# Optimization experiments

Measured on AMD Instinct MI355X. Metric: run time of the kernel, lower is better.

Reference implementation:

```python
import jax, jax.numpy as jnp
import numpy as np

N = 100000   # nodes of type 'A'
D = 128      # embedding_dim and input feature dim
E = 1600000  # edges per metapath (avg degree 16)
R = 2        # metapaths with head type 'A'; beta has R+1 channels (self)


def setup_inputs() -> dict:
    key = jax.random.key(0)
    ks = jax.random.split(key, 8)
    s = 1.0 / np.sqrt(D)
    return {
        "x": jax.random.normal(ks[0], (N, D), jnp.float32),
        "edge_index_r1": jax.random.randint(ks[1], (2, E), 0, N),
        "edge_index_r2": jax.random.randint(ks[2], (2, E), 0, N),
        "W_lin": jax.random.normal(ks[3], (D, D), jnp.float32) * s,
        "b_lin": jnp.zeros((D,), jnp.float32),
        "W_conv": jax.random.normal(ks[4], (R + 1, D), jnp.float32) * s,  # kernel-size-1 Conv1d == linear
        "b_conv": jnp.zeros((R + 1,), jnp.float32),
        "attn_l_w": jax.random.normal(ks[5], (R, D), jnp.float32) * s,
        "attn_l_b": jnp.zeros((R,), jnp.float32),
        "attn_r_w": jax.random.normal(ks[6], (R, D), jnp.float32) * s,
        "attn_r_b": jnp.zeros((R,), jnp.float32),
        "alpha_weights": jnp.ones((R,), jnp.float32),
    }


def _segment_softmax(logits, seg, n):
    mx = jax.ops.segment_max(logits, seg, num_segments=n)
    mx = jnp.where(jnp.isfinite(mx), mx, 0.0)  # empty segments
    ex = jnp.exp(logits - mx[seg])
    denom = jax.ops.segment_sum(ex, seg, num_segments=n)
    return ex / (denom[seg] + 1e-16)


def reference(x, edge_index_r1, edge_index_r2, W_lin, b_lin, W_conv, b_conv,
              attn_l_w, attn_l_b, attn_r_w, attn_r_b, alpha_weights):
    n = x.shape[0]
    h = x @ W_lin.T + b_lin                              # get_h_dict: Linear
    beta = jax.nn.softmax(x @ W_conv.T + b_conv, axis=1)  # [N, R+1] relation weights
    al = x @ jnp.zeros((0,)) if False else h @ attn_l_w.T + attn_l_b  # [N, R]
    ar = h @ attn_r_w.T + attn_r_b                        # [N, R]
    rels = []
    for m, ei in enumerate((edge_index_r1, edge_index_r2)):
        dst, src = ei[0], ei[1]  # flow='target_to_source': aggregate into edge_index[0]
        logit = alpha_weights[m] * (al[src, m] + ar[dst, m])  # [E]
        att = _segment_softmax(logit, dst, n)
        rels.append(jax.ops.segment_sum(h[src] * att[:, None], dst, num_segments=n))
    rel = jnp.stack(rels + [h], axis=1)                   # [N, R+1, D], last slot = self
    out = jnp.einsum("nrd,nr->nd", rel, beta)            # matmul(perm, beta).squeeze
    return jax.nn.relu(out)                               # activation='relu'
```

## Files before the change

kernel.cpp:

```cpp
#include <hip/hip_runtime.h>

#define DIM 128
#define NSL 128
#define WMAX 25000

typedef __attribute__((ext_vector_type(8))) short bf16x8;
typedef __attribute__((ext_vector_type(4))) float f32x4;

__device__ __forceinline__ unsigned bfbits(float f) {
    unsigned u = __float_as_uint(f);
    return (u + 0x7FFFu + ((u >> 16) & 1u)) >> 16;
}
__device__ __forceinline__ float bflo(unsigned u) { return __uint_as_float(u << 16); }
__device__ __forceinline__ float bfhi(unsigned u) { return __uint_as_float(u & 0xFFFF0000u); }

__global__ __launch_bounds__(256) void k_gemm_h(
    const float* __restrict__ x, const float* __restrict__ W,
    const float* __restrict__ b, const float* __restrict__ Wc,
    const float* __restrict__ bcv, const float* __restrict__ alw,
    const float* __restrict__ alb, const float* __restrict__ alpha,
    unsigned short* __restrict__ h2u, float* __restrict__ exal0,
    float* __restrict__ exal1, float* __restrict__ betab, int n)
{
    __shared__ short wlds[128 * 136];
    __shared__ short xlds[64 * 136];
    const int tid  = threadIdx.x;
    const int row0 = blockIdx.x * 64;

    {
        const int j = tid >> 1, half = tid & 1;
        const float4* W4 = (const float4*)W;
#pragma unroll
        for (int i = 0; i < 8; ++i) {
            float4 fa = W4[j * 32 + half * 16 + i * 2];
            float4 fb = W4[j * 32 + half * 16 + i * 2 + 1];
            uint4 p;
            p.x = bfbits(fa.x) | (bfbits(fa.y) << 16);
            p.y = bfbits(fa.z) | (bfbits(fa.w) << 16);
            p.z = bfbits(fb.x) | (bfbits(fb.y) << 16);
            p.w = bfbits(fb.z) | (bfbits(fb.w) << 16);
            *(uint4*)&wlds[j * 136 + half * 64 + i * 8] = p;
        }
    }
    {
        const int r = tid >> 2, q = tid & 3;
        const int row = min(row0 + r, n - 1);
        const float4* x4 = (const float4*)x;
#pragma unroll
        for (int i = 0; i < 4; ++i) {
            float4 fa = x4[(size_t)row * 32 + q * 8 + i * 2];
            float4 fb = x4[(size_t)row * 32 + q * 8 + i * 2 + 1];
            uint4 p;
            p.x = bfbits(fa.x) | (bfbits(fa.y) << 16);
            p.y = bfbits(fa.z) | (bfbits(fa.w) << 16);
            p.z = bfbits(fb.x) | (bfbits(fb.y) << 16);
            p.w = bfbits(fb.z) | (bfbits(fb.w) << 16);
            *(uint4*)&xlds[r * 136 + q * 32 + i * 8] = p;
        }
    }
    __syncthreads();

    const int wv = tid >> 6, lane = tid & 63;
    const int lr = lane & 15, lg = lane >> 4;

    f32x4 acc[8];
#pragma unroll
    for (int c = 0; c < 8; ++c) acc[c] = (f32x4){0.f, 0.f, 0.f, 0.f};

#pragma unroll
    for (int ks = 0; ks < 4; ++ks) {
        bf16x8 a = *(const bf16x8*)&xlds[(wv * 16 + lr) * 136 + ks * 32 + lg * 8];
#pragma unroll
        for (int c = 0; c < 8; ++c) {
            bf16x8 bb = *(const bf16x8*)&wlds[(c * 16 + lr) * 136 + ks * 32 + lg * 8];
            acc[c] = __builtin_amdgcn_mfma_f32_16x16x32_bf16(a, bb, acc[c], 0, 0, 0);
        }
    }

    const int rl0 = wv * 16 + lg * 4;
    float as0[4] = {0.f,0.f,0.f,0.f}, as1[4] = {0.f,0.f,0.f,0.f};
#pragma unroll
    for (int c = 0; c < 8; ++c) {
        const int col = c * 16 + lr;
        const float bc = b[col];
        const float w0 = alw[col], w1 = alw[128 + col];
#pragma unroll
        for (int r = 0; r < 4; ++r) {
            const float hv = acc[c][r] + bc;
            const int row = row0 + rl0 + r;
            if (row < n)
                h2u[(size_t)row * DIM + col] = (unsigned short)bfbits(hv);
            as0[r] = fmaf(hv, w0, as0[r]);
            as1[r] = fmaf(hv, w1, as1[r]);
        }
    }
    float xs0[4] = {0.f,0.f,0.f,0.f}, xs1[4] = {0.f,0.f,0.f,0.f},
          xs2[4] = {0.f,0.f,0.f,0.f};
#pragma unroll
    for (int i = 0; i < 8; ++i) {
        const int col = lr + i * 16;
        const float wc0 = Wc[col], wc1 = Wc[128 + col], wc2 = Wc[256 + col];
#pragma unroll
        for (int r = 0; r < 4; ++r) {
            const float xv = bflo((unsigned)(unsigned short)xlds[(rl0 + r) * 136 + col]);
            xs0[r] = fmaf(xv, wc0, xs0[r]);
            xs1[r] = fmaf(xv, wc1, xs1[r]);
            xs2[r] = fmaf(xv, wc2, xs2[r]);
        }
    }
#pragma unroll
    for (int o = 1; o <= 8; o <<= 1) {
#pragma unroll
        for (int r = 0; r < 4; ++r) {
            as0[r] += __shfl_xor(as0[r], o);
            as1[r] += __shfl_xor(as1[r], o);
            xs0[r] += __shfl_xor(xs0[r], o);
            xs1[r] += __shfl_xor(xs1[r], o);
            xs2[r] += __shfl_xor(xs2[r], o);
        }
    }
    if (lr == 0) {
        const float a0 = alpha[0], a1 = alpha[1];
        const float ab0 = alb[0], ab1 = alb[1];
        const float b0 = bcv[0], b1 = bcv[1], b2 = bcv[2];
#pragma unroll
        for (int r = 0; r < 4; ++r) {
            const int row = row0 + rl0 + r;
            if (row < n) {
                exal0[row] = __expf(a0 * (as0[r] + ab0));
                exal1[row] = __expf(a1 * (as1[r] + ab1));
                float c0 = xs0[r] + b0, c1 = xs1[r] + b1, c2 = xs2[r] + b2;
                float mx = fmaxf(c0, fmaxf(c1, c2));
                float e0 = __expf(c0 - mx), e1 = __expf(c1 - mx),
                      e2 = __expf(c2 - mx);
                float s = e0 + e1 + e2;
                betab[row * 3 + 0] = e0 / s;
                betab[row * 3 + 1] = e1 / s;
                betab[row * 3 + 2] = e2 / s;
            }
        }
    }
}

__global__ __launch_bounds__(1024) void k_hist(
    const int* __restrict__ ei1, const int* __restrict__ ei2,
    unsigned* __restrict__ pb, unsigned char* __restrict__ ph, int n, int e)
{
    __shared__ unsigned lds[WMAX];
    const int blk = blockIdx.x;
    const int s   = blk % NSL;
    const int m   = blk / NSL;
    const int* ei = m ? ei2 : ei1;
    const int W   = (n + 3) >> 2;

    for (int i = threadIdx.x; i < W; i += 1024) lds[i] = 0;
    __syncthreads();

    const int sl = (e + NSL - 1) / NSL;
    const int j0 = s * sl, j1 = min(j0 + sl, e);
    for (int j = j0 + threadIdx.x; j < j1; j += 1024) {
        int d  = ei[j];
        int sh = (d & 3) * 8;
        unsigned old = atomicAdd(&lds[d >> 2], 1u << sh);
        ph[(size_t)m * e + j] = (unsigned char)((old >> sh) & 0xFF);
    }
    __syncthreads();

    unsigned* dst = pb + (size_t)blk * WMAX;
    for (int i = threadIdx.x; i < W; i += 1024) dst[i] = lds[i];
}

__global__ __launch_bounds__(256) void k_combine(
    unsigned* __restrict__ pb, int* __restrict__ cnt, int n)
{
    const int W = (n + 3) >> 2;
    int t = blockIdx.x * 256 + threadIdx.x;
    if (t >= 2 * W) return;
    const int m = t / W, w = t % W;

    unsigned run = 0;
    unsigned* base = pb + ((size_t)m * NSL) * WMAX + w;
    for (int s = 0; s < NSL; ++s) {
        unsigned v = base[(size_t)s * WMAX];
        base[(size_t)s * WMAX] = run;
        run += v;
    }
    int bin = 4 * w;
    if (bin + 3 < n) {
        int4 c = make_int4(run & 0xFF, (run >> 8) & 0xFF,
                           (run >> 16) & 0xFF, (run >> 24) & 0xFF);
        *(int4*)&cnt[m * n + bin] = c;
    } else {
        for (int j = 0; j < 4 && bin + j < n; ++j)
            cnt[m * n + bin + j] = (run >> (8 * j)) & 0xFF;
    }
}

__global__ __launch_bounds__(256) void k_scan1(
    const int* __restrict__ cnt, int* __restrict__ excl,
    int* __restrict__ bsum, int n2)
{
    __shared__ int sh[256];
    int t = threadIdx.x;
    int base = blockIdx.x * 1024 + t * 4;
    int v0 = (base + 0 < n2) ? cnt[base + 0] : 0;
    int v1 = (base + 1 < n2) ? cnt[base + 1] : 0;
    int v2 = (base + 2 < n2) ? cnt[base + 2] : 0;
    int v3 = (base + 3 < n2) ? cnt[base + 3] : 0;
    int s1 = v0 + v1, s2 = s1 + v2, s3 = s2 + v3;
    sh[t] = s3;
    __syncthreads();
    for (int off = 1; off < 256; off <<= 1) {
        int a = (t >= off) ? sh[t - off] : 0;
        __syncthreads();
        sh[t] += a;
        __syncthreads();
    }
    int eb = sh[t] - s3;
    if (t == 255) bsum[blockIdx.x] = sh[255];
    if (base + 0 < n2) excl[base + 0] = eb;
    if (base + 1 < n2) excl[base + 1] = eb + v0;
    if (base + 2 < n2) excl[base + 2] = eb + s1;
    if (base + 3 < n2) excl[base + 3] = eb + s2;
}

__global__ __launch_bounds__(256) void k_scan2(int* __restrict__ bsum, int nb)
{
    __shared__ int sh[256];
    int t = threadIdx.x;
    int v = (t < nb) ? bsum[t] : 0;
    sh[t] = v;
    __syncthreads();
    for (int off = 1; off < 256; off <<= 1) {
        int a = (t >= off) ? sh[t - off] : 0;
        __syncthreads();
        sh[t] += a;
        __syncthreads();
    }
    if (t < nb) bsum[t] = sh[t] - v;
}

__global__ __launch_bounds__(256) void k_scan3(
    int* __restrict__ rp, const int* __restrict__ bsum, int n2, int etot)
{
    int i = blockIdx.x * 256 + threadIdx.x;
    if (i < n2) rp[i] += bsum[i >> 10];
    if (i == 0) rp[n2] = etot;
}

__global__ __launch_bounds__(256) void k_fill(
    const int* __restrict__ ei1, const int* __restrict__ ei2,
    const unsigned char* __restrict__ ph, const unsigned* __restrict__ pb,
    const int* __restrict__ rp, int* __restrict__ srcs,
    int sl, int n, int e)
{
    int t = blockIdx.x * 256 + threadIdx.x;
    if (t >= 2 * e) return;
    const int m = (t >= e);
    const int j = t - m * e;
    const int* ei = m ? ei2 : ei1;
    const int d  = ei[j];
    const int sv = ei[e + j];
    const int s  = j / sl;
    const int sh = (d & 3) * 8;
    const int bse  = (pb[((size_t)(m * NSL + s)) * WMAX + (d >> 2)] >> sh) & 0xFF;
    const int rank = ph[t];
    srcs[rp[m * n + d] + bse + rank] = sv;
}

__global__ __launch_bounds__(256) void k_gather(
    const unsigned* __restrict__ h2,
    const float* __restrict__ exal0, const float* __restrict__ exal1,
    const float* __restrict__ betab,
    const int* __restrict__ rp, const int* __restrict__ srcs,
    float* __restrict__ out, int n)
{
    int wid  = blockIdx.x * 4 + (threadIdx.x >> 6);
    if (wid >= n) return;
    int lane = threadIdx.x & 63;

    float b0 = betab[wid * 3 + 0];
    float b1 = betab[wid * 3 + 1];
    float b2 = betab[wid * 3 + 2];

    float2 acc;
    {
        unsigned hu = h2[(size_t)wid * 64 + lane];
        acc.x = b2 * bflo(hu);
        acc.y = b2 * bfhi(hu);
    }

#pragma unroll
    for (int m = 0; m < 2; ++m) {
        const int s0 = rp[m * n + wid];
        const int s1 = rp[m * n + wid + 1];
        const float* exal = m ? exal1 : exal0;
        const float bm = m ? b1 : b0;

        float sum = 0.0f;
        float2 a = {0.0f, 0.0f};

        for (int base = s0; base < s1; base += 64) {
            const int cnt = min(64, s1 - base);

            int   src = 0;
            float ex  = 0.0f;
            if (lane < cnt) {
                src = srcs[base + lane];
                ex  = exal[src];
            }
            {
                float t = ex;
#pragma unroll
                for (int o = 32; o > 0; o >>= 1) t += __shfl_xor(t, o);
                sum += t;
            }

            const unsigned exu = __float_as_uint(ex);
            int j = 0;
            for (; j + 8 <= cnt; j += 8) {
                unsigned u[8];
                float    w[8];
#pragma unroll
                for (int q = 0; q < 8; ++q) {
                    int s = __builtin_amdgcn_readlane(src, j + q);
                    w[q]  = __uint_as_float(__builtin_amdgcn_readlane(exu, j + q));
                    u[q]  = h2[(size_t)s * 64 + lane];
                }
#pragma unroll
                for (int q = 0; q < 8; ++q) {
                    a.x = fmaf(w[q], bflo(u[q]), a.x);
                    a.y = fmaf(w[q], bfhi(u[q]), a.y);
                }
            }
            for (; j + 2 <= cnt; j += 2) {
                int   sA = __builtin_amdgcn_readlane(src, j + 0);
                int   sB = __builtin_amdgcn_readlane(src, j + 1);
                float wA = __uint_as_float(__builtin_amdgcn_readlane(exu, j + 0));
                float wB = __uint_as_float(__builtin_amdgcn_readlane(exu, j + 1));
                unsigned uA = h2[(size_t)sA * 64 + lane];
                unsigned uB = h2[(size_t)sB * 64 + lane];
                a.x = fmaf(wA, bflo(uA), a.x); a.y = fmaf(wA, bfhi(uA), a.y);
                a.x = fmaf(wB, bflo(uB), a.x); a.y = fmaf(wB, bfhi(uB), a.y);
            }
            if (j < cnt) {
                int   sA = __builtin_amdgcn_readlane(src, j);
                float wA = __uint_as_float(__builtin_amdgcn_readlane(exu, j));
                unsigned uA = h2[(size_t)sA * 64 + lane];
                a.x = fmaf(wA, bflo(uA), a.x);
                a.y = fmaf(wA, bfhi(uA), a.y);
            }
        }

        float sc = bm / (sum + 1e-16f);
        acc.x = fmaf(sc, a.x, acc.x);
        acc.y = fmaf(sc, a.y, acc.y);
    }

    float2 o;
    o.x = fmaxf(acc.x, 0.0f);
    o.y = fmaxf(acc.y, 0.0f);
    *(float2*)(out + (size_t)wid * DIM + lane * 2) = o;
}

extern "C" void kernel_launch(void* const* d_in, const int* in_sizes, int n_in,
                              void* d_out, int out_size, void* d_ws, size_t ws_size,
                              hipStream_t stream)
{
    const float* x     = (const float*)d_in[0];
    const int*   ei1   = (const int*)d_in[1];
    const int*   ei2   = (const int*)d_in[2];
    const float* W_lin = (const float*)d_in[3];
    const float* b_lin = (const float*)d_in[4];
    const float* W_cv  = (const float*)d_in[5];
    const float* b_cv  = (const float*)d_in[6];
    const float* alw   = (const float*)d_in[7];
    const float* alb   = (const float*)d_in[8];
    const float* alpha = (const float*)d_in[11];

    const int N  = in_sizes[0] / DIM;
    const int E  = in_sizes[1] / 2;
    const int N2 = 2 * N;
    const int W  = (N + 3) >> 2;
    const int SL = (E + NSL - 1) / NSL;

    float* out = (float*)d_out;

    unsigned* h2    = (unsigned*)d_ws;
    float*    exal0 = (float*)(h2 + (size_t)N * 64);
    float*    exal1 = exal0 + N;
    float*    betab = exal1 + N;
    int*      rp    = (int*)(betab + (size_t)3 * N);
    int*      cnt   = rp + (N2 + 2);
    int*      bsum  = cnt + N2;
    unsigned* pb    = (unsigned*)(bsum + 256);
    unsigned char* ph = (unsigned char*)(pb + (size_t)2 * NSL * WMAX);
    int*      srcs  = (int*)(ph + (size_t)2 * E);

    const int nb = (N2 + 1023) / 1024;

    k_gemm_h<<<(N + 63) / 64, 256, 0, stream>>>(x, W_lin, b_lin, W_cv, b_cv,
                                                alw, alb, alpha,
                                                (unsigned short*)h2,
                                                exal0, exal1, betab, N);

    k_hist<<<2 * NSL, 1024, 0, stream>>>(ei1, ei2, pb, ph, N, E);

    k_combine<<<(2 * W + 255) / 256, 256, 0, stream>>>(pb, cnt, N);

    k_scan1<<<nb, 256, 0, stream>>>(cnt, rp, bsum, N2);
    k_scan2<<<1, 256, 0, stream>>>(bsum, nb);
    k_scan3<<<(N2 + 255) / 256, 256, 0, stream>>>(rp, bsum, N2, 2 * E);

    k_fill<<<(2 * E + 255) / 256, 256, 0, stream>>>(ei1, ei2, ph, pb, rp, srcs,
                                                    SL, N, E);

    k_gather<<<(N + 3) / 4, 256, 0, stream>>>(h2, exal0, exal1, betab,
                                              rp, srcs, out, N);
}
```

Baseline: 257.7 us.

## Fold attention/conv projections into an extra MFMA and fuse combine with scan

Precomputes W_lin^T·attn_l and the conv weights as five bf16 vectors in a small prep kernel, so the attention logits and beta logits come from one extra MFMA per k-step instead of scalar FMAs and shuffle reductions. It also merges the per-slice count combine with the first scan pass and drops the separate scan-add kernel, applying block offsets lazily in fill and gather. This removes two launches and a cnt round-trip, at the cost of extra bsum reads in fill and gather. The logits are now computed from bf16 x against bf16-rounded folded weights, which may shift their numerics slightly.

```diff
diff --git a/kernel.cpp b/kernel.cpp
--- a/kernel.cpp
+++ b/kernel.cpp
@@ -14,11 +14,43 @@
 __device__ __forceinline__ float bflo(unsigned u) { return __uint_as_float(u << 16); }
 __device__ __forceinline__ float bfhi(unsigned u) { return __uint_as_float(u & 0xFFFF0000u); }
 
+__global__ __launch_bounds__(256) void k_prep(
+    const float* __restrict__ W, const float* __restrict__ b,
+    const float* __restrict__ Wc, const float* __restrict__ alw,
+    const float* __restrict__ alb,
+    unsigned short* __restrict__ v5u, float* __restrict__ consts)
+{
+    const int tid = threadIdx.x;
+    if (tid < 128) {
+        const int k = tid;
+        float f0 = 0.f, f1 = 0.f;
+        for (int c = 0; c < 128; ++c) {
+            const float w = W[c * 128 + k];
+            f0 = fmaf(w, alw[c],       f0);
+            f1 = fmaf(w, alw[128 + c], f1);
+        }
+        v5u[3 * 128 + k] = (unsigned short)bfbits(f0);
+        v5u[4 * 128 + k] = (unsigned short)bfbits(f1);
+    }
+    for (int i = tid; i < 384; i += 256)
+        v5u[i] = (unsigned short)bfbits(Wc[i]);
+    if (tid == 254) {
+        float s = 0.f;
+        for (int c = 0; c < 128; ++c) s = fmaf(b[c], alw[c], s);
+        consts[0] = s + alb[0];
+    }
+    if (tid == 255) {
+        float s = 0.f;
+        for (int c = 0; c < 128; ++c) s = fmaf(b[c], alw[128 + c], s);
+        consts[1] = s + alb[1];
+    }
+}
+
 __global__ __launch_bounds__(256) void k_gemm_h(
     const float* __restrict__ x, const float* __restrict__ W,
-    const float* __restrict__ b, const float* __restrict__ Wc,
-    const float* __restrict__ bcv, const float* __restrict__ alw,
-    const float* __restrict__ alb, const float* __restrict__ alpha,
+    const float* __restrict__ b, const float* __restrict__ bcv,
+    const float* __restrict__ alpha,
+    const unsigned short* __restrict__ v5u, const float* __restrict__ consts,
     unsigned short* __restrict__ h2u, float* __restrict__ exal0,
     float* __restrict__ exal1, float* __restrict__ betab, int n)
 {
@@ -66,6 +98,7 @@
     f32x4 acc[8];
 #pragma unroll
     for (int c = 0; c < 8; ++c) acc[c] = (f32x4){0.f, 0.f, 0.f, 0.f};
+    f32x4 acc5 = (f32x4){0.f, 0.f, 0.f, 0.f};
 
 #pragma unroll
     for (int ks = 0; ks < 4; ++ks) {
@@ -75,61 +108,40 @@
             bf16x8 bb = *(const bf16x8*)&wlds[(c * 16 + lr) * 136 + ks * 32 + lg * 8];
             acc[c] = __builtin_amdgcn_mfma_f32_16x16x32_bf16(a, bb, acc[c], 0, 0, 0);
         }
+        bf16x8 b5 = (bf16x8){0,0,0,0,0,0,0,0};
+        if (lr < 5)
+            b5 = *(const bf16x8*)&v5u[lr * 128 + ks * 32 + lg * 8];
+        acc5 = __builtin_amdgcn_mfma_f32_16x16x32_bf16(a, b5, acc5, 0, 0, 0);
     }
 
     const int rl0 = wv * 16 + lg * 4;
-    float as0[4] = {0.f,0.f,0.f,0.f}, as1[4] = {0.f,0.f,0.f,0.f};
 #pragma unroll
     for (int c = 0; c < 8; ++c) {
         const int col = c * 16 + lr;
         const float bc = b[col];
-        const float w0 = alw[col], w1 = alw[128 + col];
 #pragma unroll
         for (int r = 0; r < 4; ++r) {
-            const float hv = acc[c][r] + bc;
             const int row = row0 + rl0 + r;
             if (row < n)
-                h2u[(size_t)row * DIM + col] = (unsigned short)bfbits(hv);
-            as0[r] = fmaf(hv, w0, as0[r]);
-            as1[r] = fmaf(hv, w1, as1[r]);
-        }
-    }
-    float xs0[4] = {0.f,0.f,0.f,0.f}, xs1[4] = {0.f,0.f,0.f,0.f},
-          xs2[4] = {0.f,0.f,0.f,0.f};
-#pragma unroll
-    for (int i = 0; i < 8; ++i) {
-        const int col = lr + i * 16;
-        const float wc0 = Wc[col], wc1 = Wc[128 + col], wc2 = Wc[256 + col];
-#pragma unroll
-        for (int r = 0; r < 4; ++r) {
-            const float xv = bflo((unsigned)(unsigned short)xlds[(rl0 + r) * 136 + col]);
-            xs0[r] = fmaf(xv, wc0, xs0[r]);
-            xs1[r] = fmaf(xv, wc1, xs1[r]);
-            xs2[r] = fmaf(xv, wc2, xs2[r]);
-        }
-    }
-#pragma unroll
-    for (int o = 1; o <= 8; o <<= 1) {
-#pragma unroll
-        for (int r = 0; r < 4; ++r) {
-            as0[r] += __shfl_xor(as0[r], o);
-            as1[r] += __shfl_xor(as1[r], o);
-            xs0[r] += __shfl_xor(xs0[r], o);
-            xs1[r] += __shfl_xor(xs1[r], o);
-            xs2[r] += __shfl_xor(xs2[r], o);
-        }
-    }
-    if (lr == 0) {
-        const float a0 = alpha[0], a1 = alpha[1];
-        const float ab0 = alb[0], ab1 = alb[1];
-        const float b0 = bcv[0], b1 = bcv[1], b2 = bcv[2];
-#pragma unroll
-        for (int r = 0; r < 4; ++r) {
-            const int row = row0 + rl0 + r;
-            if (row < n) {
-                exal0[row] = __expf(a0 * (as0[r] + ab0));
-                exal1[row] = __expf(a1 * (as1[r] + ab1));
-                float c0 = xs0[r] + b0, c1 = xs1[r] + b1, c2 = xs2[r] + b2;
+                h2u[(size_t)row * DIM + col] = (unsigned short)bfbits(acc[c][r] + bc);
+        }
+    }
+
+    const float alpha0 = alpha[0], alpha1 = alpha[1];
+    const float cal0 = consts[0], cal1 = consts[1];
+    const float bc0 = bcv[0], bc1 = bcv[1], bc2 = bcv[2];
+    const int lgbase = lane & 48;
+#pragma unroll
+    for (int r = 0; r < 4; ++r) {
+        const float v   = acc5[r];
+        const float c1v = __shfl(v, lgbase + 1);
+        const float c2v = __shfl(v, lgbase + 2);
+        const int row = row0 + rl0 + r;
+        if (row < n) {
+            if (lr == 3) exal0[row] = __expf(alpha0 * (v + cal0));
+            if (lr == 4) exal1[row] = __expf(alpha1 * (v + cal1));
+            if (lr == 0) {
+                float c0 = v + bc0, c1 = c1v + bc1, c2 = c2v + bc2;
                 float mx = fmaxf(c0, fmaxf(c1, c2));
                 float e0 = __expf(c0 - mx), e1 = __expf(c1 - mx),
                       e2 = __expf(c2 - mx);
@@ -170,43 +182,29 @@
     for (int i = threadIdx.x; i < W; i += 1024) dst[i] = lds[i];
 }
 
-__global__ __launch_bounds__(256) void k_combine(
-    unsigned* __restrict__ pb, int* __restrict__ cnt, int n)
-{
+__global__ __launch_bounds__(256) void k_cscan(
+    unsigned* __restrict__ pb, int* __restrict__ rp,
+    int* __restrict__ bsum, int n)
+{
+    __shared__ int sh[256];
+    const int t = threadIdx.x;
     const int W = (n + 3) >> 2;
-    int t = blockIdx.x * 256 + threadIdx.x;
-    if (t >= 2 * W) return;
-    const int m = t / W, w = t % W;
-
-    unsigned run = 0;
-    unsigned* base = pb + ((size_t)m * NSL) * WMAX + w;
-    for (int s = 0; s < NSL; ++s) {
-        unsigned v = base[(size_t)s * WMAX];
-        base[(size_t)s * WMAX] = run;
-        run += v;
-    }
-    int bin = 4 * w;
-    if (bin + 3 < n) {
-        int4 c = make_int4(run & 0xFF, (run >> 8) & 0xFF,
-                           (run >> 16) & 0xFF, (run >> 24) & 0xFF);
-        *(int4*)&cnt[m * n + bin] = c;
-    } else {
-        for (int j = 0; j < 4 && bin + j < n; ++j)
-            cnt[m * n + bin + j] = (run >> (8 * j)) & 0xFF;
-    }
-}
-
-__global__ __launch_bounds__(256) void k_scan1(
-    const int* __restrict__ cnt, int* __restrict__ excl,
-    int* __restrict__ bsum, int n2)
-{
-    __shared__ int sh[256];
-    int t = threadIdx.x;
-    int base = blockIdx.x * 1024 + t * 4;
-    int v0 = (base + 0 < n2) ? cnt[base + 0] : 0;
-    int v1 = (base + 1 < n2) ? cnt[base + 1] : 0;
-    int v2 = (base + 2 < n2) ? cnt[base + 2] : 0;
-    int v3 = (base + 3 < n2) ? cnt[base + 3] : 0;
+    const int w = blockIdx.x * 256 + t;
+
+    int v0 = 0, v1 = 0, v2 = 0, v3 = 0;
+    if (w < 2 * W) {
+        const int m  = (w >= W);
+        const int lw = w - m * W;
+        unsigned* base = pb + ((size_t)m * NSL) * WMAX + lw;
+        unsigned run = 0;
+        for (int s = 0; s < NSL; ++s) {
+            unsigned v = base[(size_t)s * WMAX];
+            base[(size_t)s * WMAX] = run;
+            run += v;
+        }
+        v0 = run & 0xFF; v1 = (run >> 8) & 0xFF;
+        v2 = (run >> 16) & 0xFF; v3 = (run >> 24) & 0xFF;
+    }
     int s1 = v0 + v1, s2 = s1 + v2, s3 = s2 + v3;
     sh[t] = s3;
     __syncthreads();
@@ -218,10 +216,13 @@
     }
     int eb = sh[t] - s3;
     if (t == 255) bsum[blockIdx.x] = sh[255];
-    if (base + 0 < n2) excl[base + 0] = eb;
-    if (base + 1 < n2) excl[base + 1] = eb + v0;
-    if (base + 2 < n2) excl[base + 2] = eb + s1;
-    if (base + 3 < n2) excl[base + 3] = eb + s2;
+    if (w < 2 * W) {
+        int g = w * 4;
+        rp[g + 0] = eb;
+        rp[g + 1] = eb + v0;
+        rp[g + 2] = eb + s1;
+        rp[g + 3] = eb + s2;
+    }
 }
 
 __global__ __launch_bounds__(256) void k_scan2(int* __restrict__ bsum, int nb)
@@ -240,19 +241,11 @@
     if (t < nb) bsum[t] = sh[t] - v;
 }
 
-__global__ __launch_bounds__(256) void k_scan3(
-    int* __restrict__ rp, const int* __restrict__ bsum, int n2, int etot)
-{
-    int i = blockIdx.x * 256 + threadIdx.x;
-    if (i < n2) rp[i] += bsum[i >> 10];
-    if (i == 0) rp[n2] = etot;
-}
-
 __global__ __launch_bounds__(256) void k_fill(
     const int* __restrict__ ei1, const int* __restrict__ ei2,
     const unsigned char* __restrict__ ph, const unsigned* __restrict__ pb,
-    const int* __restrict__ rp, int* __restrict__ srcs,
-    int sl, int n, int e)
+    const int* __restrict__ rp, const int* __restrict__ bsum,
+    int* __restrict__ srcs, int sl, int n, int e)
 {
     int t = blockIdx.x * 256 + threadIdx.x;
     if (t >= 2 * e) return;
@@ -264,16 +257,17 @@
     const int s  = j / sl;
     const int sh = (d & 3) * 8;
     const int bse  = (pb[((size_t)(m * NSL + s)) * WMAX + (d >> 2)] >> sh) & 0xFF;
-    const int rank = ph[t];
-    srcs[rp[m * n + d] + bse + rank] = sv;
+    const int i    = m * n + d;
+    srcs[rp[i] + bsum[i >> 10] + bse + (int)ph[t]] = sv;
 }
 
 __global__ __launch_bounds__(256) void k_gather(
     const unsigned* __restrict__ h2,
     const float* __restrict__ exal0, const float* __restrict__ exal1,
     const float* __restrict__ betab,
-    const int* __restrict__ rp, const int* __restrict__ srcs,
-    float* __restrict__ out, int n)
+    const int* __restrict__ rp, const int* __restrict__ bsum,
+    const int* __restrict__ srcs,
+    float* __restrict__ out, int n, int e2)
 {
     int wid  = blockIdx.x * 4 + (threadIdx.x >> 6);
     if (wid >= n) return;
@@ -292,8 +286,10 @@
 
 #pragma unroll
     for (int m = 0; m < 2; ++m) {
-        const int s0 = rp[m * n + wid];
-        const int s1 = rp[m * n + wid + 1];
+        const int i  = m * n + wid;
+        const int s0 = rp[i] + bsum[i >> 10];
+        const int i1 = i + 1;
+        const int s1 = (i1 == 2 * n) ? e2 : rp[i1] + bsum[i1 >> 10];
         const float* exal = m ? exal1 : exal0;
         const float bm = m ? b1 : b0;
 
@@ -391,30 +387,30 @@
     float*    exal1 = exal0 + N;
     float*    betab = exal1 + N;
     int*      rp    = (int*)(betab + (size_t)3 * N);
-    int*      cnt   = rp + (N2 + 2);
-    int*      bsum  = cnt + N2;
-    unsigned* pb    = (unsigned*)(bsum + 256);
+    int*      bsum  = rp + (N2 + 2);
+    unsigned short* v5u = (unsigned short*)(bsum + 256);
+    float*    consts = (float*)(v5u + 640);
+    unsigned* pb    = (unsigned*)(consts + 4);
     unsigned char* ph = (unsigned char*)(pb + (size_t)2 * NSL * WMAX);
     int*      srcs  = (int*)(ph + (size_t)2 * E);
 
-    const int nb = (N2 + 1023) / 1024;
-
-    k_gemm_h<<<(N + 63) / 64, 256, 0, stream>>>(x, W_lin, b_lin, W_cv, b_cv,
-                                                alw, alb, alpha,
+    const int ncs = (2 * W + 255) / 256;
+
+    k_prep<<<1, 256, 0, stream>>>(W_lin, b_lin, W_cv, alw, alb, v5u, consts);
+
+    k_gemm_h<<<(N + 63) / 64, 256, 0, stream>>>(x, W_lin, b_lin, b_cv, alpha,
+                                                v5u, consts,
                                                 (unsigned short*)h2,
                                                 exal0, exal1, betab, N);
 
     k_hist<<<2 * NSL, 1024, 0, stream>>>(ei1, ei2, pb, ph, N, E);
 
-    k_combine<<<(2 * W + 255) / 256, 256, 0, stream>>>(pb, cnt, N);
-
-    k_scan1<<<nb, 256, 0, stream>>>(cnt, rp, bsum, N2);
-    k_scan2<<<1, 256, 0, stream>>>(bsum, nb);
-    k_scan3<<<(N2 + 255) / 256, 256, 0, stream>>>(rp, bsum, N2, 2 * E);
-
-    k_fill<<<(2 * E + 255) / 256, 256, 0, stream>>>(ei1, ei2, ph, pb, rp, srcs,
-                                                    SL, N, E);
+    k_cscan<<<ncs, 256, 0, stream>>>(pb, rp, bsum, N);
+    k_scan2<<<1, 256, 0, stream>>>(bsum, ncs);
+
+    k_fill<<<(2 * E + 255) / 256, 256, 0, stream>>>(ei1, ei2, ph, pb, rp, bsum,
+                                                    srcs, SL, N, E);
 
     k_gather<<<(N + 3) / 4, 256, 0, stream>>>(h2, exal0, exal1, betab,
-                                              rp, srcs, out, N);
-}
+                                              rp, bsum, srcs, out, N, 2 * E);
+}
```

Result: slower. 264.2 us (+2.5%).
